# Kernel tuning notes

Hardware: AMD Instinct MI355X
Metric: run time of the kernel (lower is better)

Reference implementation:

```python
import jax, jax.numpy as jnp
import numpy as np

N_NODES = 50000
N_EDGES = 1250000
D_IN = 256
D_OUT = 64


def setup_inputs() -> dict:
    key = jax.random.key(0)
    k0, k1, k2, k3, k4 = jax.random.split(key, 5)
    return {
        "arg0_1": jax.random.normal(k0, (D_OUT, D_IN), dtype=jnp.float32),
        "arg1_1": jax.random.normal(k1, (D_OUT,), dtype=jnp.float32),
        "arg2_1": jax.random.randint(k2, (2, N_EDGES), 0, N_NODES, dtype=jnp.int64),
        "arg3_1": jax.random.uniform(k3, (N_EDGES,), dtype=jnp.float32),
        "arg4_1": jax.random.normal(k4, (N_NODES, D_IN), dtype=jnp.float32),
    }


def reference(arg0_1, arg1_1, arg2_1, arg3_1, arg4_1):
    # h = x @ W^T  : [N, D_OUT]
    h = jnp.matmul(arg4_1, arg0_1.T)
    src = arg2_1[0]  # gather indices
    dst = arg2_1[1]  # scatter_add indices
    # edge messages: gather source rows, scale by edge weight  : [E, D_OUT]
    msg = arg3_1[:, None] * h[src]
    # scatter_add into node buckets
    agg = jax.ops.segment_sum(msg, dst, num_segments=N_NODES)
    return agg + arg1_1
```

## Files before the change

### kernel.cpp

```cpp
#include <hip/hip_runtime.h>
#include <hip/hip_bf16.h>

#define D_IN    256
#define D_OUT   64
#define NNODES  50000
#define NEDGES  1250000

#define BUCK_SHIFT 8
#define BUCK_NODES 256
#define NBUCK      196
#define CPAD       16
#define EPB        4096
#define NB_EDGE    ((NEDGES + EPB - 1) / EPB)
#define GEMM_BLOCKS ((NNODES + 63) / 64)
#define BCAP    8128

typedef float f32x4 __attribute__((ext_vector_type(4)));
typedef short s16x8 __attribute__((ext_vector_type(8)));

static __device__ __forceinline__ unsigned short f2bf(float f) {
    union { float f; unsigned u; } v; v.f = f;
    unsigned r = v.u + 0x7FFFu + ((v.u >> 16) & 1u);
    return (unsigned short)(r >> 16);
}

__global__ __launch_bounds__(256) void gemm_bin(
    const float* __restrict__ x, const float* __restrict__ W,
    signed char* __restrict__ hq, float* __restrict__ scale_tab, int N,
    const int* __restrict__ src, const int* __restrict__ dst,
    const float* __restrict__ wt,
    int* __restrict__ bcursor, unsigned long long* __restrict__ binned)
{
    __shared__ uint4 sW[2048];
    __shared__ int   lcnt[NBUCK];
    __shared__ int   lbase[NBUCK];

    const int t = threadIdx.x;

    if (blockIdx.x >= GEMM_BLOCKS) {
        for (int i = t; i < NBUCK; i += 256) lcnt[i] = 0;
        __syncthreads();

        int base = (blockIdx.x - GEMM_BLOCKS) * EPB;
        bool full = (base + EPB <= NEDGES);

        if (full) {
            const int4* d4 = (const int4*)(dst + base);
            #pragma unroll
            for (int it = 0; it < 4; ++it) {
                int4 d = d4[t + it * 256];
                atomicAdd(&lcnt[d.x >> BUCK_SHIFT], 1);
                atomicAdd(&lcnt[d.y >> BUCK_SHIFT], 1);
                atomicAdd(&lcnt[d.z >> BUCK_SHIFT], 1);
                atomicAdd(&lcnt[d.w >> BUCK_SHIFT], 1);
            }
        } else {
            for (int e = base + t; e < NEDGES; e += 256)
                atomicAdd(&lcnt[dst[e] >> BUCK_SHIFT], 1);
        }
        __syncthreads();

        if (t < NBUCK) {
            int c = lcnt[t];
            lbase[t] = c ? (t * BCAP + atomicAdd(&bcursor[t * CPAD], c)) : 0;
            lcnt[t]  = 0;
        }
        __syncthreads();

        if (full) {
            const int4*   s4 = (const int4*)(src + base);
            const int4*   d4 = (const int4*)(dst + base);
            const float4* w4 = (const float4*)(wt + base);
            #pragma unroll
            for (int it = 0; it < 4; ++it) {
                int4   ss = s4[t + it * 256];
                int4   dd = d4[t + it * 256];
                float4 ww = w4[t + it * 256];
                int sv[4]   = {ss.x, ss.y, ss.z, ss.w};
                int dv[4]   = {dd.x, dd.y, dd.z, dd.w};
                float wv[4] = {ww.x, ww.y, ww.z, ww.w};
                #pragma unroll
                for (int k = 0; k < 4; ++k) {
                    int d = dv[k];
                    int b = d >> BUCK_SHIFT;
                    int r = atomicAdd(&lcnt[b], 1);
                    unsigned lo = (unsigned)sv[k] | ((unsigned)(d & (BUCK_NODES - 1)) << 16);
                    unsigned long long rec = (unsigned long long)lo
                                           | ((unsigned long long)__float_as_uint(wv[k]) << 32);
                    binned[lbase[b] + r] = rec;
                }
            }
        } else {
            for (int e = base + t; e < NEDGES; e += 256) {
                int d = dst[e];
                int b = d >> BUCK_SHIFT;
                int r = atomicAdd(&lcnt[b], 1);
                int sidx = src[e];
                unsigned lo = (unsigned)sidx | ((unsigned)(d & (BUCK_NODES - 1)) << 16);
                unsigned long long rec = (unsigned long long)lo
                                       | ((unsigned long long)__float_as_uint(wt[e]) << 32);
                binned[lbase[b] + r] = rec;
            }
        }
        return;
    }

    const int lane = t & 63;
    const int wave = t >> 6;
    const int m    = lane & 15;
    const int q    = lane >> 4;

    #pragma unroll
    for (int i = 0; i < 8; ++i) {
        int slot = t + i * 256;
        int ln   = slot & 63;
        int kb   = (slot >> 6) & 7;
        int c    = slot >> 9;
        int lm = ln & 15, lq = ln >> 4;
        const float* wp = W + (c * 16 + lm) * D_IN + kb * 32 + lq * 8;
        float4 w0 = *(const float4*)wp;
        float4 w1 = *(const float4*)(wp + 4);
        uint4 u;
        u.x = (unsigned)f2bf(w0.x) | ((unsigned)f2bf(w0.y) << 16);
        u.y = (unsigned)f2bf(w0.z) | ((unsigned)f2bf(w0.w) << 16);
        u.z = (unsigned)f2bf(w1.x) | ((unsigned)f2bf(w1.y) << 16);
        u.w = (unsigned)f2bf(w1.z) | ((unsigned)f2bf(w1.w) << 16);
        sW[slot] = u;
    }
    __syncthreads();

    const int rowA = blockIdx.x * 64 + wave * 16 + m;
    const int rowc = (rowA < N) ? rowA : (N - 1);
    const float* xr = x + (long long)rowc * D_IN + q * 8;

    f32x4 acc[4] = {};

    #pragma unroll
    for (int kb = 0; kb < 8; ++kb) {
        float4 a0 = *(const float4*)(xr + kb * 32);
        float4 a1 = *(const float4*)(xr + kb * 32 + 4);
        s16x8 af;
        af[0] = (short)f2bf(a0.x); af[1] = (short)f2bf(a0.y);
        af[2] = (short)f2bf(a0.z); af[3] = (short)f2bf(a0.w);
        af[4] = (short)f2bf(a1.x); af[5] = (short)f2bf(a1.y);
        af[6] = (short)f2bf(a1.z); af[7] = (short)f2bf(a1.w);

        #pragma unroll
        for (int c = 0; c < 4; ++c) {
            s16x8 bf = *(const s16x8*)&sW[(c * 8 + kb) * 64 + lane];
            acc[c] = __builtin_amdgcn_mfma_f32_16x16x32_bf16(af, bf, acc[c], 0, 0, 0);
        }
    }

    #pragma unroll
    for (int r = 0; r < 4; ++r) {
        float local = fmaxf(fmaxf(fabsf(acc[0][r]), fabsf(acc[1][r])),
                            fmaxf(fabsf(acc[2][r]), fabsf(acc[3][r])));
        #pragma unroll
        for (int msk = 1; msk < 16; msk <<= 1)
            local = fmaxf(local, __shfl_xor(local, msk));
        float amax = fmaxf(local, 1e-6f);
        float inv  = 127.0f / amax;
        int gr = blockIdx.x * 64 + wave * 16 + q * 4 + r;
        if (gr < N) {
            if (m == 0) scale_tab[gr] = amax * (1.0f / 127.0f);
            #pragma unroll
            for (int c = 0; c < 4; ++c) {
                int qv = __float2int_rn(acc[c][r] * inv);
                hq[(long long)gr * D_OUT + c * 16 + m] = (signed char)qv;
            }
        }
    }
}

__global__ __launch_bounds__(512) void sort_buckets(
    const unsigned long long* __restrict__ binned, const int* __restrict__ bcursor,
    const float* __restrict__ scale_tab,
    unsigned long long* __restrict__ csr,
    int* __restrict__ starts, int* __restrict__ counts)
{
    __shared__ int s[256];
    __shared__ int lcnt[BUCK_NODES];
    __shared__ int lcur[BUCK_NODES];
    __shared__ int sh_s0, sh_cnt;
    int t = threadIdx.x;
    int b = blockIdx.x;

    const unsigned long long* bsrc = binned + (long long)b * BCAP;
    unsigned long long rv[16];
    #pragma unroll
    for (int j = 0; j < 16; ++j) {
        int k = t + j * 512;
        rv[j] = (k < BCAP) ? bsrc[k] : 0ULL;
    }

    int v = 0;
    if (t < 256) {
        v = (t < NBUCK) ? bcursor[t * CPAD] : 0;
        s[t] = v;
        lcnt[t] = 0;
    }
    __syncthreads();
    #pragma unroll
    for (int off = 1; off < 256; off <<= 1) {
        int u = (t < 256 && t >= off) ? s[t - off] : 0;
        __syncthreads();
        if (t < 256) s[t] += u;
        __syncthreads();
    }
    if (t == b) { sh_s0 = s[t] - v; sh_cnt = v; }
    __syncthreads();
    int s0 = sh_s0, cntb = sh_cnt;
    int node0 = b << BUCK_SHIFT;
    int nn = min(BUCK_NODES, NNODES - node0);

    #pragma unroll
    for (int j = 0; j < 16; ++j) {
        int k = t + j * 512;
        if (k < cntb)
            atomicAdd(&lcnt[(int)((rv[j] >> 16) & 0xFF)], 1);
    }
    __syncthreads();

    int v2 = 0;
    if (t < 256) { v2 = lcnt[t]; s[t] = v2; }
    __syncthreads();
    #pragma unroll
    for (int off = 1; off < 256; off <<= 1) {
        int u = (t < 256 && t >= off) ? s[t - off] : 0;
        __syncthreads();
        if (t < 256) s[t] += u;
        __syncthreads();
    }
    if (t < 256) {
        int excl = s[t] - v2;
        lcur[t] = s0 + excl;
        if (t < nn) {
            starts[node0 + t] = s0 + excl;
            counts[node0 + t] = v2;
        }
    }
    __syncthreads();

    #pragma unroll
    for (int j = 0; j < 16; ++j) {
        int k = t + j * 512;
        if (k < cntb) {
            unsigned long long r = rv[j];
            int dloc = (int)((r >> 16) & 0xFF);
            int sidx = (int)(r & 0xFFFF);
            float wf = __uint_as_float((unsigned)(r >> 32)) * scale_tab[sidx];
            int pos  = atomicAdd(&lcur[dloc], 1);
            csr[pos] = (r & 0xFFFFFFFFull)
                     | ((unsigned long long)__float_as_uint(wf) << 32);
        }
    }
}

__global__ __launch_bounds__(256) void agg_nodes(
    const int2* __restrict__ recs, const int* __restrict__ starts,
    const int* __restrict__ counts, const signed char* __restrict__ hq,
    const float* __restrict__ bias, float* __restrict__ out)
{
    int wid  = (blockIdx.x * 256 + threadIdx.x) >> 6;
    int node = __builtin_amdgcn_readfirstlane(wid);
    if (node >= NNODES) return;
    int lane = threadIdx.x & 63;

    float acc = bias[lane];
    int s0  = starts[node];
    int cnt = counts[node];
    int i = s0, e = s0 + cnt;

    for (; i + 7 < e; i += 8) {
        int2 r0 = recs[i + 0];
        int2 r1 = recs[i + 1];
        int2 r2 = recs[i + 2];
        int2 r3 = recs[i + 3];
        int2 r4 = recs[i + 4];
        int2 r5 = recs[i + 5];
        int2 r6 = recs[i + 6];
        int2 r7 = recs[i + 7];
        float v0 = (float)hq[(r0.x & 0xFFFF) * D_OUT + lane];
        float v1 = (float)hq[(r1.x & 0xFFFF) * D_OUT + lane];
        float v2 = (float)hq[(r2.x & 0xFFFF) * D_OUT + lane];
        float v3 = (float)hq[(r3.x & 0xFFFF) * D_OUT + lane];
        float v4 = (float)hq[(r4.x & 0xFFFF) * D_OUT + lane];
        float v5 = (float)hq[(r5.x & 0xFFFF) * D_OUT + lane];
        float v6 = (float)hq[(r6.x & 0xFFFF) * D_OUT + lane];
        float v7 = (float)hq[(r7.x & 0xFFFF) * D_OUT + lane];
        acc += __int_as_float(r0.y) * v0;
        acc += __int_as_float(r1.y) * v1;
        acc += __int_as_float(r2.y) * v2;
        acc += __int_as_float(r3.y) * v3;
        acc += __int_as_float(r4.y) * v4;
        acc += __int_as_float(r5.y) * v5;
        acc += __int_as_float(r6.y) * v6;
        acc += __int_as_float(r7.y) * v7;
    }
    for (; i + 3 < e; i += 4) {
        int2 r0 = recs[i + 0];
        int2 r1 = recs[i + 1];
        int2 r2 = recs[i + 2];
        int2 r3 = recs[i + 3];
        float v0 = (float)hq[(r0.x & 0xFFFF) * D_OUT + lane];
        float v1 = (float)hq[(r1.x & 0xFFFF) * D_OUT + lane];
        float v2 = (float)hq[(r2.x & 0xFFFF) * D_OUT + lane];
        float v3 = (float)hq[(r3.x & 0xFFFF) * D_OUT + lane];
        acc += __int_as_float(r0.y) * v0;
        acc += __int_as_float(r1.y) * v1;
        acc += __int_as_float(r2.y) * v2;
        acc += __int_as_float(r3.y) * v3;
    }
    for (; i < e; ++i) {
        int2 r = recs[i];
        acc += __int_as_float(r.y) * (float)hq[(r.x & 0xFFFF) * D_OUT + lane];
    }
    out[(long long)node * D_OUT + lane] = acc;
}

__global__ __launch_bounds__(256) void init_bias(
    float* __restrict__ out, const float* __restrict__ bias, int total)
{
    int i = blockIdx.x * blockDim.x + threadIdx.x;
    if (i < total) out[i] = bias[i & (D_OUT - 1)];
}

__global__ __launch_bounds__(256) void scatter_edges(
    const int* __restrict__ src, const int* __restrict__ dst,
    const float* __restrict__ wt, const signed char* __restrict__ hq,
    const float* __restrict__ scale_tab, float* __restrict__ out)
{
    long long gid = (long long)blockIdx.x * blockDim.x + threadIdx.x;
    int e    = (int)(gid >> 6);
    int lane = threadIdx.x & 63;
    if (e < NEDGES) {
        int   s = src[e];
        int   d = dst[e];
        float w = wt[e] * scale_tab[s];
        float v = w * (float)hq[(long long)s * D_OUT + lane];
        atomicAdd(&out[(long long)d * D_OUT + lane], v);
    }
}

extern "C" void kernel_launch(void* const* d_in, const int* in_sizes, int n_in,
                              void* d_out, int out_size, void* d_ws, size_t ws_size,
                              hipStream_t stream)
{
    const float* W     = (const float*)d_in[0];
    const float* bias  = (const float*)d_in[1];
    const int*   edges = (const int*)  d_in[2];
    const float* wt    = (const float*)d_in[3];
    const float* x     = (const float*)d_in[4];
    float*       out   = (float*)d_out;

    const int* src = edges;
    const int* dst = edges + NEDGES;

    char* ws = (char*)d_ws;
    const size_t OFF_HQ     = 0;
    const size_t OFF_SCALE  = 3200000;
    const size_t OFF_RECS   = 3400000;
    const size_t OFF_STARTS = 13400000;
    const size_t OFF_COUNTS = 13600000;
    const size_t OFF_BCUR   = 13800000;
    const size_t REQUIRED   = 13812544;

    signed char* hq        = (signed char*)(ws + OFF_HQ);
    float*       scale_tab = (float*)(ws + OFF_SCALE);

    if (ws_size >= REQUIRED) {
        unsigned long long* csr     = (unsigned long long*)(ws + OFF_RECS);
        int*                starts  = (int*)(ws + OFF_STARTS);
        int*                counts  = (int*)(ws + OFF_COUNTS);
        int*                bcursor = (int*)(ws + OFF_BCUR);

        unsigned long long* binned = (unsigned long long*)d_out;

        hipMemsetAsync(bcursor, 0, NBUCK * CPAD * sizeof(int), stream);

        gemm_bin<<<GEMM_BLOCKS + NB_EDGE, 256, 0, stream>>>(
            x, W, hq, scale_tab, NNODES, src, dst, wt, bcursor, binned);

        sort_buckets<<<NBUCK, 512, 0, stream>>>(binned, bcursor, scale_tab,
                                                csr, starts, counts);

        int nb = (NNODES * 64 + 255) / 256;
        agg_nodes<<<nb, 256, 0, stream>>>((const int2*)csr, starts, counts,
                                          hq, bias, out);
    } else {
        gemm_bin<<<GEMM_BLOCKS, 256, 0, stream>>>(
            x, W, hq, scale_tab, NNODES,
            (const int*)nullptr, (const int*)nullptr, (const float*)nullptr,
            (int*)nullptr, (unsigned long long*)nullptr);
        int total = NNODES * D_OUT;
        init_bias<<<(total + 255) / 256, 256, 0, stream>>>(out, bias, total);
        long long threads = (long long)NEDGES * 64;
        int blocks = (int)((threads + 255) / 256);
        scatter_edges<<<blocks, 256, 0, stream>>>(src, dst, wt, hq, scale_tab, out);
    }
}
```

Before: 168.2 us.

## Fuse bucket sort and node aggregation into one kernel using shared-memory records

The per-bucket sort and the per-node aggregation now run in one kernel. Each block sorts its bucket's edge records into a shared-memory array and then aggregates its nodes directly from it. This removes the global CSR buffer, the starts/counts arrays and a kernel launch. Buckets are halved to 128 nodes so a bucket's records fit in LDS, which doubles the block count and launches more atomics on the cursors. The output buffer doubles as the binned staging area, so a block's output writes can overlap the start of the next bucket's staging data and race with that block's reads if it has not yet loaded them.

```diff
diff --git a/kernel.cpp b/kernel.cpp
--- a/kernel.cpp
+++ b/kernel.cpp
@@ -6,14 +6,14 @@
 #define NNODES  50000
 #define NEDGES  1250000
 
-#define BUCK_SHIFT 8
-#define BUCK_NODES 256
-#define NBUCK      196
+#define BUCK_SHIFT 7
+#define BUCK_NODES 128
+#define NBUCK      391
 #define CPAD       16
 #define EPB        4096
 #define NB_EDGE    ((NEDGES + EPB - 1) / EPB)
 #define GEMM_BLOCKS ((NNODES + 63) / 64)
-#define BCAP    8128
+#define BCAP    4092
 
 typedef float f32x4 __attribute__((ext_vector_type(4)));
 typedef short s16x8 __attribute__((ext_vector_type(8)));
@@ -60,10 +60,10 @@
         }
         __syncthreads();
 
-        if (t < NBUCK) {
-            int c = lcnt[t];
-            lbase[t] = c ? (t * BCAP + atomicAdd(&bcursor[t * CPAD], c)) : 0;
-            lcnt[t]  = 0;
+        for (int i = t; i < NBUCK; i += 256) {
+            int c = lcnt[i];
+            lbase[i] = c ? (i * BCAP + atomicAdd(&bcursor[i * CPAD], c)) : 0;
+            lcnt[i]  = 0;
         }
         __syncthreads();
 
@@ -173,49 +173,33 @@
     }
 }
 
-__global__ __launch_bounds__(512) void sort_buckets(
+__global__ __launch_bounds__(512) void sortagg(
     const unsigned long long* __restrict__ binned, const int* __restrict__ bcursor,
-    const float* __restrict__ scale_tab,
-    unsigned long long* __restrict__ csr,
-    int* __restrict__ starts, int* __restrict__ counts)
-{
+    const float* __restrict__ scale_tab, const signed char* __restrict__ hq,
+    const float* __restrict__ bias, float* __restrict__ out)
+{
+    __shared__ unsigned long long srt[BCAP];
     __shared__ int s[256];
     __shared__ int lcnt[BUCK_NODES];
+    __shared__ int lstart[BUCK_NODES];
     __shared__ int lcur[BUCK_NODES];
-    __shared__ int sh_s0, sh_cnt;
-    int t = threadIdx.x;
-    int b = blockIdx.x;
+    const int t = threadIdx.x;
+    const int b = blockIdx.x;
 
     const unsigned long long* bsrc = binned + (long long)b * BCAP;
-    unsigned long long rv[16];
-    #pragma unroll
-    for (int j = 0; j < 16; ++j) {
+    unsigned long long rv[8];
+    #pragma unroll
+    for (int j = 0; j < 8; ++j) {
         int k = t + j * 512;
         rv[j] = (k < BCAP) ? bsrc[k] : 0ULL;
     }
 
-    int v = 0;
-    if (t < 256) {
-        v = (t < NBUCK) ? bcursor[t * CPAD] : 0;
-        s[t] = v;
-        lcnt[t] = 0;
-    }
-    __syncthreads();
-    #pragma unroll
-    for (int off = 1; off < 256; off <<= 1) {
-        int u = (t < 256 && t >= off) ? s[t - off] : 0;
-        __syncthreads();
-        if (t < 256) s[t] += u;
-        __syncthreads();
-    }
-    if (t == b) { sh_s0 = s[t] - v; sh_cnt = v; }
-    __syncthreads();
-    int s0 = sh_s0, cntb = sh_cnt;
-    int node0 = b << BUCK_SHIFT;
-    int nn = min(BUCK_NODES, NNODES - node0);
-
-    #pragma unroll
-    for (int j = 0; j < 16; ++j) {
+    const int cntb = bcursor[b * CPAD];
+    if (t < BUCK_NODES) lcnt[t] = 0;
+    __syncthreads();
+
+    #pragma unroll
+    for (int j = 0; j < 8; ++j) {
         int k = t + j * 512;
         if (k < cntb)
             atomicAdd(&lcnt[(int)((rv[j] >> 16) & 0xFF)], 1);
@@ -223,7 +207,7 @@
     __syncthreads();
 
     int v2 = 0;
-    if (t < 256) { v2 = lcnt[t]; s[t] = v2; }
+    if (t < 256) { v2 = (t < BUCK_NODES) ? lcnt[t] : 0; s[t] = v2; }
     __syncthreads();
     #pragma unroll
     for (int off = 1; off < 256; off <<= 1) {
@@ -232,18 +216,15 @@
         if (t < 256) s[t] += u;
         __syncthreads();
     }
-    if (t < 256) {
+    if (t < BUCK_NODES) {
         int excl = s[t] - v2;
-        lcur[t] = s0 + excl;
-        if (t < nn) {
-            starts[node0 + t] = s0 + excl;
-            counts[node0 + t] = v2;
-        }
-    }
-    __syncthreads();
-
-    #pragma unroll
-    for (int j = 0; j < 16; ++j) {
+        lstart[t] = excl;
+        lcur[t]   = excl;
+    }
+    __syncthreads();
+
+    #pragma unroll
+    for (int j = 0; j < 8; ++j) {
         int k = t + j * 512;
         if (k < cntb) {
             unsigned long long r = rv[j];
@@ -251,72 +232,73 @@
             int sidx = (int)(r & 0xFFFF);
             float wf = __uint_as_float((unsigned)(r >> 32)) * scale_tab[sidx];
             int pos  = atomicAdd(&lcur[dloc], 1);
-            csr[pos] = (r & 0xFFFFFFFFull)
+            srt[pos] = (r & 0xFFFFFFFFull)
                      | ((unsigned long long)__float_as_uint(wf) << 32);
         }
     }
-}
-
-__global__ __launch_bounds__(256) void agg_nodes(
-    const int2* __restrict__ recs, const int* __restrict__ starts,
-    const int* __restrict__ counts, const signed char* __restrict__ hq,
-    const float* __restrict__ bias, float* __restrict__ out)
-{
-    int wid  = (blockIdx.x * 256 + threadIdx.x) >> 6;
-    int node = __builtin_amdgcn_readfirstlane(wid);
-    if (node >= NNODES) return;
-    int lane = threadIdx.x & 63;
-
-    float acc = bias[lane];
-    int s0  = starts[node];
-    int cnt = counts[node];
-    int i = s0, e = s0 + cnt;
-
-    for (; i + 7 < e; i += 8) {
-        int2 r0 = recs[i + 0];
-        int2 r1 = recs[i + 1];
-        int2 r2 = recs[i + 2];
-        int2 r3 = recs[i + 3];
-        int2 r4 = recs[i + 4];
-        int2 r5 = recs[i + 5];
-        int2 r6 = recs[i + 6];
-        int2 r7 = recs[i + 7];
-        float v0 = (float)hq[(r0.x & 0xFFFF) * D_OUT + lane];
-        float v1 = (float)hq[(r1.x & 0xFFFF) * D_OUT + lane];
-        float v2 = (float)hq[(r2.x & 0xFFFF) * D_OUT + lane];
-        float v3 = (float)hq[(r3.x & 0xFFFF) * D_OUT + lane];
-        float v4 = (float)hq[(r4.x & 0xFFFF) * D_OUT + lane];
-        float v5 = (float)hq[(r5.x & 0xFFFF) * D_OUT + lane];
-        float v6 = (float)hq[(r6.x & 0xFFFF) * D_OUT + lane];
-        float v7 = (float)hq[(r7.x & 0xFFFF) * D_OUT + lane];
-        acc += __int_as_float(r0.y) * v0;
-        acc += __int_as_float(r1.y) * v1;
-        acc += __int_as_float(r2.y) * v2;
-        acc += __int_as_float(r3.y) * v3;
-        acc += __int_as_float(r4.y) * v4;
-        acc += __int_as_float(r5.y) * v5;
-        acc += __int_as_float(r6.y) * v6;
-        acc += __int_as_float(r7.y) * v7;
-    }
-    for (; i + 3 < e; i += 4) {
-        int2 r0 = recs[i + 0];
-        int2 r1 = recs[i + 1];
-        int2 r2 = recs[i + 2];
-        int2 r3 = recs[i + 3];
-        float v0 = (float)hq[(r0.x & 0xFFFF) * D_OUT + lane];
-        float v1 = (float)hq[(r1.x & 0xFFFF) * D_OUT + lane];
-        float v2 = (float)hq[(r2.x & 0xFFFF) * D_OUT + lane];
-        float v3 = (float)hq[(r3.x & 0xFFFF) * D_OUT + lane];
-        acc += __int_as_float(r0.y) * v0;
-        acc += __int_as_float(r1.y) * v1;
-        acc += __int_as_float(r2.y) * v2;
-        acc += __int_as_float(r3.y) * v3;
-    }
-    for (; i < e; ++i) {
-        int2 r = recs[i];
-        acc += __int_as_float(r.y) * (float)hq[(r.x & 0xFFFF) * D_OUT + lane];
-    }
-    out[(long long)node * D_OUT + lane] = acc;
+    __syncthreads();
+
+    const int lane  = t & 63;
+    const int wave  = t >> 6;
+    const int node0 = b << BUCK_SHIFT;
+    const int nn    = min(BUCK_NODES, NNODES - node0);
+    const float bv  = bias[lane];
+
+    for (int jj = 0; jj < 16; ++jj) {
+        int n = wave * 16 + jj;
+        if (n >= nn) break;
+        float acc = 0.0f;
+        int st  = lstart[n];
+        int cnt = lcnt[n];
+        int i = st, e = st + cnt;
+
+        for (; i + 7 < e; i += 8) {
+            unsigned long long q0 = srt[i + 0];
+            unsigned long long q1 = srt[i + 1];
+            unsigned long long q2 = srt[i + 2];
+            unsigned long long q3 = srt[i + 3];
+            unsigned long long q4 = srt[i + 4];
+            unsigned long long q5 = srt[i + 5];
+            unsigned long long q6 = srt[i + 6];
+            unsigned long long q7 = srt[i + 7];
+            float v0 = (float)hq[(int)(q0 & 0xFFFF) * D_OUT + lane];
+            float v1 = (float)hq[(int)(q1 & 0xFFFF) * D_OUT + lane];
+            float v2_ = (float)hq[(int)(q2 & 0xFFFF) * D_OUT + lane];
+            float v3 = (float)hq[(int)(q3 & 0xFFFF) * D_OUT + lane];
+            float v4 = (float)hq[(int)(q4 & 0xFFFF) * D_OUT + lane];
+            float v5 = (float)hq[(int)(q5 & 0xFFFF) * D_OUT + lane];
+            float v6 = (float)hq[(int)(q6 & 0xFFFF) * D_OUT + lane];
+            float v7 = (float)hq[(int)(q7 & 0xFFFF) * D_OUT + lane];
+            acc += __uint_as_float((unsigned)(q0 >> 32)) * v0;
+            acc += __uint_as_float((unsigned)(q1 >> 32)) * v1;
+            acc += __uint_as_float((unsigned)(q2 >> 32)) * v2_;
+            acc += __uint_as_float((unsigned)(q3 >> 32)) * v3;
+            acc += __uint_as_float((unsigned)(q4 >> 32)) * v4;
+            acc += __uint_as_float((unsigned)(q5 >> 32)) * v5;
+            acc += __uint_as_float((unsigned)(q6 >> 32)) * v6;
+            acc += __uint_as_float((unsigned)(q7 >> 32)) * v7;
+        }
+        for (; i + 3 < e; i += 4) {
+            unsigned long long q0 = srt[i + 0];
+            unsigned long long q1 = srt[i + 1];
+            unsigned long long q2 = srt[i + 2];
+            unsigned long long q3 = srt[i + 3];
+            float v0 = (float)hq[(int)(q0 & 0xFFFF) * D_OUT + lane];
+            float v1 = (float)hq[(int)(q1 & 0xFFFF) * D_OUT + lane];
+            float v2_ = (float)hq[(int)(q2 & 0xFFFF) * D_OUT + lane];
+            float v3 = (float)hq[(int)(q3 & 0xFFFF) * D_OUT + lane];
+            acc += __uint_as_float((unsigned)(q0 >> 32)) * v0;
+            acc += __uint_as_float((unsigned)(q1 >> 32)) * v1;
+            acc += __uint_as_float((unsigned)(q2 >> 32)) * v2_;
+            acc += __uint_as_float((unsigned)(q3 >> 32)) * v3;
+        }
+        for (; i < e; ++i) {
+            unsigned long long q = srt[i];
+            acc += __uint_as_float((unsigned)(q >> 32))
+                 * (float)hq[(int)(q & 0xFFFF) * D_OUT + lane];
+        }
+        out[(long long)(node0 + n) * D_OUT + lane] = acc + bv;
+    }
 }
 
 __global__ __launch_bounds__(256) void init_bias(
@@ -360,20 +342,14 @@
     char* ws = (char*)d_ws;
     const size_t OFF_HQ     = 0;
     const size_t OFF_SCALE  = 3200000;
-    const size_t OFF_RECS   = 3400000;
-    const size_t OFF_STARTS = 13400000;
-    const size_t OFF_COUNTS = 13600000;
-    const size_t OFF_BCUR   = 13800000;
-    const size_t REQUIRED   = 13812544;
+    const size_t OFF_BCUR   = 3400000;
+    const size_t REQUIRED   = 3425024;
 
     signed char* hq        = (signed char*)(ws + OFF_HQ);
     float*       scale_tab = (float*)(ws + OFF_SCALE);
 
     if (ws_size >= REQUIRED) {
-        unsigned long long* csr     = (unsigned long long*)(ws + OFF_RECS);
-        int*                starts  = (int*)(ws + OFF_STARTS);
-        int*                counts  = (int*)(ws + OFF_COUNTS);
-        int*                bcursor = (int*)(ws + OFF_BCUR);
+        int* bcursor = (int*)(ws + OFF_BCUR);
 
         unsigned long long* binned = (unsigned long long*)d_out;
 
@@ -382,12 +358,8 @@
         gemm_bin<<<GEMM_BLOCKS + NB_EDGE, 256, 0, stream>>>(
             x, W, hq, scale_tab, NNODES, src, dst, wt, bcursor, binned);
 
-        sort_buckets<<<NBUCK, 512, 0, stream>>>(binned, bcursor, scale_tab,
-                                                csr, starts, counts);
-
-        int nb = (NNODES * 64 + 255) / 256;
-        agg_nodes<<<nb, 256, 0, stream>>>((const int2*)csr, starts, counts,
-                                          hq, bias, out);
+        sortagg<<<NBUCK, 512, 0, stream>>>(binned, bcursor, scale_tab,
+                                           hq, bias, out);
     } else {
         gemm_bin<<<GEMM_BLOCKS, 256, 0, stream>>>(
             x, W, hq, scale_tab, NNODES,
```

Measured after the change: 168.9 us. No clear change (+0.4%).
